# Kernel optimization log

Measured on AMD Instinct MI355X. Metric: run time of the kernel, lower is better.

## Reference

```python
import jax, jax.numpy as jnp
import numpy as np

N_NODES = 1_000_000
N_EDGES = 16_000_000
F_IN, F_H1, F_H2, N_CLS = 32, 16, 8, 5
N_GRAPHS = 10_000


def setup_inputs() -> dict:
    key = jax.random.key(0)
    ks = jax.random.split(key, 10)
    x = jax.random.normal(ks[0], (N_NODES, F_IN), dtype=jnp.float32)
    edge_index = jax.random.randint(ks[1], (2, N_EDGES), 0, N_NODES, dtype=jnp.int32)
    batch = jnp.sort(jax.random.randint(ks[2], (N_NODES,), 0, N_GRAPHS, dtype=jnp.int32))
    # learned params (Glorot-ish scale)
    W1 = jax.random.normal(ks[3], (F_IN, F_H1), dtype=jnp.float32) / np.sqrt(F_IN)
    b1 = jnp.zeros((F_H1,), dtype=jnp.float32)
    W2 = jax.random.normal(ks[4], (F_H1, F_H2), dtype=jnp.float32) / np.sqrt(F_H1)
    b2 = jnp.zeros((F_H2,), dtype=jnp.float32)
    Wl = jax.random.normal(ks[5], (F_H2, N_CLS), dtype=jnp.float32) / np.sqrt(F_H2)
    bl = jnp.zeros((N_CLS,), dtype=jnp.float32)
    return {"x": x, "edge_index": edge_index, "batch": batch, "num_graphs": N_GRAPHS,
            "W1": W1, "b1": b1, "W2": W2, "b2": b2, "Wl": Wl, "bl": bl}


def _gcn_conv(x, W, b, src, dst, deg_inv_sqrt, norm_e, num_nodes):
    # h = X W, then symmetric-normalized aggregation with self loops:
    # out_i = sum_{(j->i)} norm_ji * h_j + deg_i^{-1} * h_i + b
    h = x @ W                                  # [N, F_out]
    msg = h[src] * norm_e[:, None]             # [E, F_out] gather + scale
    agg = jax.ops.segment_sum(msg, dst, num_segments=num_nodes)
    self_loop = h * (deg_inv_sqrt * deg_inv_sqrt)[:, None]
    return agg + self_loop + b


def reference(x, edge_index, batch, num_graphs, W1, b1, W2, b2, Wl, bl):
    num_nodes = x.shape[0]
    src, dst = edge_index[0], edge_index[1]
    # degrees including self loops (GCN: A_hat = A + I)
    deg = jax.ops.segment_sum(jnp.ones_like(dst, dtype=x.dtype), dst,
                              num_segments=num_nodes) + 1.0
    deg_inv_sqrt = jax.lax.rsqrt(deg)
    norm_e = deg_inv_sqrt[src] * deg_inv_sqrt[dst]   # [E]

    h = _gcn_conv(x, W1, b1, src, dst, deg_inv_sqrt, norm_e, num_nodes)
    h = jax.nn.relu(h)
    h = _gcn_conv(h, W2, b2, src, dst, deg_inv_sqrt, norm_e, num_nodes)
    h = jax.nn.relu(h)

    # global_mean_pool over graph ids
    sums = jax.ops.segment_sum(h, batch, num_segments=num_graphs)     # [G, F_H2]
    cnts = jax.ops.segment_sum(jnp.ones((num_nodes,), dtype=h.dtype), batch,
                               num_segments=num_graphs)
    pooled = sums / jnp.maximum(cnts, 1.0)[:, None]
    return pooled @ Wl + bl
```

## Files before the change

kernel.cpp:

```cpp
#include <hip/hip_runtime.h>


namespace {

constexpr int F_IN = 32, F_H1 = 16, F_H2 = 8, N_CLS = 5;
constexpr int BB = 10, NPB = 1 << BB;
constexpr int MAXB = 1024;
constexpr int CHUNK = 12288;


__global__ void k_mm1(const float* __restrict__ x, const float* __restrict__ W,
                      float* __restrict__ h, int N) {
  __shared__ float w[F_IN * F_H1];
  for (int k = threadIdx.x; k < F_IN * F_H1; k += blockDim.x) w[k] = W[k];
  __syncthreads();
  int i = blockIdx.x * blockDim.x + threadIdx.x;
  if (i >= N) return;
  const float4* xr = reinterpret_cast<const float4*>(x + (size_t)i * F_IN);
  float acc[F_H1];
#pragma unroll
  for (int f = 0; f < F_H1; ++f) acc[f] = 0.f;
#pragma unroll
  for (int k4 = 0; k4 < F_IN / 4; ++k4) {
    float4 v = xr[k4];
    float vv[4] = {v.x, v.y, v.z, v.w};
#pragma unroll
    for (int j = 0; j < 4; ++j) {
      const float* wr = &w[(k4 * 4 + j) * F_H1];
#pragma unroll
      for (int f = 0; f < F_H1; ++f) acc[f] = fmaf(vv[j], wr[f], acc[f]);
    }
  }
  float4* hr = reinterpret_cast<float4*>(h + (size_t)i * F_H1);
#pragma unroll
  for (int q = 0; q < F_H1 / 4; ++q)
    hr[q] = make_float4(acc[q * 4], acc[q * 4 + 1], acc[q * 4 + 2], acc[q * 4 + 3]);
}

__global__ void k_mm2(const float* __restrict__ in, const float* __restrict__ W,
                      float* __restrict__ h, int N) {
  __shared__ float w[F_H1 * F_H2];
  for (int k = threadIdx.x; k < F_H1 * F_H2; k += blockDim.x) w[k] = W[k];
  __syncthreads();
  int i = blockIdx.x * blockDim.x + threadIdx.x;
  if (i >= N) return;
  const float4* xr = reinterpret_cast<const float4*>(in + (size_t)i * F_H1);
  float acc[F_H2];
#pragma unroll
  for (int f = 0; f < F_H2; ++f) acc[f] = 0.f;
#pragma unroll
  for (int k4 = 0; k4 < F_H1 / 4; ++k4) {
    float4 v = xr[k4];
    float vv[4] = {v.x, v.y, v.z, v.w};
#pragma unroll
    for (int j = 0; j < 4; ++j) {
      const float* wr = &w[(k4 * 4 + j) * F_H2];
#pragma unroll
      for (int f = 0; f < F_H2; ++f) acc[f] = fmaf(vv[j], wr[f], acc[f]);
    }
  }
  float4* hr = reinterpret_cast<float4*>(h + (size_t)i * F_H2);
#pragma unroll
  for (int q = 0; q < F_H2 / 4; ++q)
    hr[q] = make_float4(acc[q * 4], acc[q * 4 + 1], acc[q * 4 + 2], acc[q * 4 + 3]);
}

__global__ void k_final(const float* __restrict__ pooled, const float* __restrict__ cnts,
                        const float* __restrict__ Wl, const float* __restrict__ bl,
                        float* __restrict__ out, int total) {
  int gid = blockIdx.x * blockDim.x + threadIdx.x;
  if (gid >= total) return;
  int g = gid / N_CLS, c = gid % N_CLS;
  float s = 0.f;
#pragma unroll
  for (int f = 0; f < F_H2; ++f) s += pooled[g * F_H2 + f] * Wl[f * N_CLS + c];
  out[gid] = s / fmaxf(cnts[g], 1.f) + bl[c];
}


__global__ void k_hist(const int* __restrict__ dst, int* __restrict__ bcnt,
                       int E, int nbuck) {
  __shared__ int h[MAXB];
  for (int i = threadIdx.x; i < MAXB; i += blockDim.x) h[i] = 0;
  __syncthreads();
  for (int e = blockIdx.x * blockDim.x + threadIdx.x; e < E;
       e += gridDim.x * blockDim.x)
    atomicAdd(&h[dst[e] >> BB], 1);
  __syncthreads();
  for (int i = threadIdx.x; i < nbuck; i += blockDim.x)
    if (h[i]) atomicAdd(&bcnt[i], h[i]);
}

__global__ void k_bscan(const int* __restrict__ bcnt, int* __restrict__ bbase,
                        int* __restrict__ bcur, int nbuck, int E) {
  __shared__ int s[MAXB];
  int t = threadIdx.x;
  int v = (t < nbuck) ? bcnt[t] : 0;
  s[t] = v;
  __syncthreads();
  for (int off = 1; off < MAXB; off <<= 1) {
    int x = (t >= off) ? s[t - off] : 0;
    __syncthreads();
    s[t] += x;
    __syncthreads();
  }
  int ex = s[t] - v;
  if (t < nbuck) { bbase[t] = ex; bcur[t] = ex; }
  if (t == 0) bbase[nbuck] = E;
}

__global__ __launch_bounds__(256)
void k_binscatter(const int* __restrict__ dst, const int* __restrict__ src,
                  int* __restrict__ bcur, int* __restrict__ packed, int E) {
  __shared__ int hist[MAXB];
  __shared__ int sbase[MAXB];
  __shared__ int lcur[MAXB];
  __shared__ int stg[CHUNK];
  __shared__ int stmp[256];
  int t = threadIdx.x;
  int c0 = blockIdx.x * CHUNK;
  int n = min(CHUNK, E - c0);
  for (int i = t; i < MAXB; i += 256) hist[i] = 0;
  __syncthreads();
  for (int j = t; j < n; j += 256) atomicAdd(&hist[dst[c0 + j] >> BB], 1);
  __syncthreads();
  int v[4], sum = 0;
  int b4 = t * 4;
#pragma unroll
  for (int k = 0; k < 4; ++k) { v[k] = hist[b4 + k]; sum += v[k]; }
  stmp[t] = sum;
  __syncthreads();
  for (int off = 1; off < 256; off <<= 1) {
    int x = (t >= off) ? stmp[t - off] : 0;
    __syncthreads();
    stmp[t] += x;
    __syncthreads();
  }
  int run = stmp[t] - sum;
#pragma unroll
  for (int k = 0; k < 4; ++k) { sbase[b4 + k] = run; lcur[b4 + k] = run; run += v[k]; }
  __syncthreads();
  for (int i = t; i < MAXB; i += 256) {
    int c = hist[i];
    if (c) hist[i] = atomicAdd(&bcur[i], c);
  }
  __syncthreads();
  for (int j = t; j < n; j += 256) {
    int d = dst[c0 + j], s = src[c0 + j];
    int b = d >> BB;
    int p = atomicAdd(&lcur[b], 1);
    stg[p] = ((d & (NPB - 1)) << 20) | s;
  }
  __syncthreads();
  for (int j = t; j < n; j += 256) {
    int lo = 0, hi = MAXB - 1;
    while (lo < hi) {
      int mid = (lo + hi + 1) >> 1;
      if (sbase[mid] <= j) lo = mid; else hi = mid - 1;
    }
    packed[hist[lo] + (j - sbase[lo])] = stg[j];
  }
}

__global__ void k_dis_b(const int* __restrict__ bbase, const int* __restrict__ packed,
                        float* __restrict__ dis, int N) {
  __shared__ int cnt[NPB];
  int t = threadIdx.x;
  for (int i = t; i < NPB; i += blockDim.x) cnt[i] = 0;
  __syncthreads();
  int b = blockIdx.x;
  int beg = bbase[b], end = bbase[b + 1];
  for (int e = beg + t; e < end; e += blockDim.x)
    atomicAdd(&cnt[packed[e] >> 20], 1);
  __syncthreads();
  int node0 = b << BB;
  for (int i = t; i < NPB; i += blockDim.x) {
    int node = node0 + i;
    if (node < N) dis[node] = rsqrtf((float)cnt[i] + 1.0f);
  }
}


template <int F>
__global__ __launch_bounds__(512)
void k_conv(const int* __restrict__ bbase, const int* __restrict__ packed,
            const float* __restrict__ dis, const float* __restrict__ h,
            const float* __restrict__ bias, float* __restrict__ out, int N) {
  __shared__ float acc[NPB * F];
  int t = threadIdx.x;
  for (int i = t; i < NPB * F; i += 512) acc[i] = 0.f;
  __syncthreads();
  int b = blockIdx.x;
  int beg = bbase[b], end = bbase[b + 1];
  const int EPI = 512 / F;
  int f = t % F, eg = t / F;
  for (int e = beg + eg; e < end; e += 2 * EPI) {
    int p0 = packed[e];
    int s0 = p0 & ((1 << 20) - 1), d0 = p0 >> 20;
    float m0 = dis[s0] * h[(size_t)s0 * F + f];
    int e1 = e + EPI;
    if (e1 < end) {
      int p1 = packed[e1];
      int s1 = p1 & ((1 << 20) - 1), d1 = p1 >> 20;
      float m1 = dis[s1] * h[(size_t)s1 * F + f];
      atomicAdd(&acc[d0 * F + f], m0);
      atomicAdd(&acc[d1 * F + f], m1);
    } else {
      atomicAdd(&acc[d0 * F + f], m0);
    }
  }
  __syncthreads();
  int node0 = b << BB;
  for (int i = t; i < NPB * F; i += 512) {
    int node = node0 + i / F;
    if (node >= N) continue;
    int ff = i % F;
    float di = dis[node];
    float v = fmaf(di, acc[i], fmaf(di * di, h[(size_t)node * F + ff], bias[ff]));
    out[(size_t)node * F + ff] = fmaxf(v, 0.f);
  }
}

__global__ __launch_bounds__(512)
void k_conv_pool(const int* __restrict__ bbase, const int* __restrict__ packed,
                 const float* __restrict__ dis, const float* __restrict__ h,
                 const float* __restrict__ bias, const int* __restrict__ batch,
                 float* __restrict__ pooled, float* __restrict__ cnts, int N) {
  constexpr int F = F_H2;
  __shared__ float acc[NPB * F];
  int t = threadIdx.x;
  for (int i = t; i < NPB * F; i += 512) acc[i] = 0.f;
  __syncthreads();
  int b = blockIdx.x;
  int beg = bbase[b], end = bbase[b + 1];
  const int EPI = 512 / F;
  int f = t % F, eg = t / F;
  for (int e = beg + eg; e < end; e += 2 * EPI) {
    int p0 = packed[e];
    int s0 = p0 & ((1 << 20) - 1), d0 = p0 >> 20;
    float m0 = dis[s0] * h[(size_t)s0 * F + f];
    int e1 = e + EPI;
    if (e1 < end) {
      int p1 = packed[e1];
      int s1 = p1 & ((1 << 20) - 1), d1 = p1 >> 20;
      float m1 = dis[s1] * h[(size_t)s1 * F + f];
      atomicAdd(&acc[d0 * F + f], m0);
      atomicAdd(&acc[d1 * F + f], m1);
    } else {
      atomicAdd(&acc[d0 * F + f], m0);
    }
  }
  __syncthreads();
  int node0 = b << BB;
  for (int i = t; i < NPB * F; i += 512) {
    int node = node0 + i / F;
    if (node >= N) continue;
    int ff = i % F;
    float di = dis[node];
    float v = fmaf(di, acc[i], fmaf(di * di, h[(size_t)node * F + ff], bias[ff]));
    v = fmaxf(v, 0.f);
    int g = batch[node];
    atomicAdd(&pooled[g * F_H2 + ff], v);
    if (ff == 0) atomicAdd(&cnts[g], 1.0f);
  }
}


__global__ void k_deg(const int* __restrict__ dst, float* __restrict__ deg, int E) {
  int e = blockIdx.x * blockDim.x + threadIdx.x;
  if (e < E) atomicAdd(&deg[dst[e]], 1.0f);
}
__global__ void k_dis(float* __restrict__ d, int N) {
  int i = blockIdx.x * blockDim.x + threadIdx.x;
  if (i < N) d[i] = rsqrtf(d[i] + 1.0f);
}
template <int F>
__global__ void k_edge(const int* __restrict__ src, const int* __restrict__ dst,
                       const float* __restrict__ dis, const float* __restrict__ h,
                       float* __restrict__ agg, int total) {
  int gid = blockIdx.x * blockDim.x + threadIdx.x;
  if (gid >= total) return;
  int e = gid / F, f = gid % F;
  int s = src[e], d = dst[e];
  atomicAdd(&agg[d * F + f], h[s * F + f] * dis[s] * dis[d]);
}
template <int F>
__global__ void k_combine(const float* __restrict__ h, const float* __restrict__ dis,
                          const float* __restrict__ b, float* __restrict__ agg, int total) {
  int gid = blockIdx.x * blockDim.x + threadIdx.x;
  if (gid >= total) return;
  int i = gid / F, f = gid % F;
  float di = dis[i];
  agg[gid] = fmaxf(agg[gid] + h[gid] * di * di + b[f], 0.f);
}
__global__ void k_combine_pool_fb(const float* __restrict__ h2, const float* __restrict__ agg2,
                                  const float* __restrict__ dis, const float* __restrict__ b,
                                  const int* __restrict__ batch, float* __restrict__ pooled,
                                  float* __restrict__ cnts, int total) {
  int gid = blockIdx.x * blockDim.x + threadIdx.x;
  if (gid >= total) return;
  int i = gid >> 3, f = gid & 7;
  float di = dis[i];
  float v = fmaxf(agg2[gid] + h2[gid] * di * di + b[f], 0.f);
  int g = batch[i];
  atomicAdd(&pooled[g * F_H2 + f], v);
  if (f == 0) atomicAdd(&cnts[g], 1.0f);
}

}

extern "C" void kernel_launch(void* const* d_in, const int* in_sizes, int n_in,
                              void* d_out, int out_size, void* d_ws, size_t ws_size,
                              hipStream_t stream) {
  const float* x   = (const float*)d_in[0];
  const int* ei    = (const int*)d_in[1];
  const int* batch = (const int*)d_in[2];
  const float* W1 = (const float*)d_in[4];
  const float* b1 = (const float*)d_in[5];
  const float* W2 = (const float*)d_in[6];
  const float* b2 = (const float*)d_in[7];
  const float* Wl = (const float*)d_in[8];
  const float* bl = (const float*)d_in[9];

  const int N = in_sizes[0] / F_IN;
  const int E = in_sizes[1] / 2;
  const int G = out_size / N_CLS;
  const int* src  = ei;
  const int* dstp = ei + E;

  const int BLK = 256;
  const int nbuck = (N + NPB - 1) >> BB;

  size_t need = (size_t)(3 * MAXB + 8) * 4
              + (size_t)E * 4
              + (size_t)N * 4
              + (size_t)N * F_H1 * 4
              + (size_t)N * F_H1 * 4
              + (size_t)G * (F_H2 + 1) * 4 + 1024;

  if (N <= (1 << 20) && nbuck <= MAXB && ws_size >= need) {
    char* p = (char*)d_ws;
    int*   bcnt   = (int*)p;    p += (size_t)MAXB * 4;
    int*   bbase  = (int*)p;    p += (size_t)(MAXB + 4) * 4;
    int*   bcur   = (int*)p;    p += (size_t)MAXB * 4;
    int*   packed = (int*)p;    p += (size_t)E * 4;
    float* dis    = (float*)p;  p += (size_t)N * 4;
    float* H      = (float*)p;  p += (size_t)N * F_H1 * 4;
    float* O      = (float*)p;  p += (size_t)N * F_H1 * 4;
    float* pooled = (float*)p;  p += (size_t)G * F_H2 * 4;
    float* cnts   = (float*)p;

    hipMemsetAsync(bcnt, 0, (size_t)MAXB * 4, stream);
    hipMemsetAsync(pooled, 0, ((size_t)G * F_H2 + G) * 4, stream);

    k_hist<<<2048, BLK, 0, stream>>>(dstp, bcnt, E, nbuck);
    k_bscan<<<1, MAXB, 0, stream>>>(bcnt, bbase, bcur, nbuck, E);
    k_binscatter<<<(E + CHUNK - 1) / CHUNK, BLK, 0, stream>>>(dstp, src, bcur, packed, E);
    k_dis_b<<<nbuck, BLK, 0, stream>>>(bbase, packed, dis, N);

    k_mm1<<<(N + BLK - 1) / BLK, BLK, 0, stream>>>(x, W1, H, N);
    k_conv<F_H1><<<nbuck, 512, 0, stream>>>(bbase, packed, dis, H, b1, O, N);
    k_mm2<<<(N + BLK - 1) / BLK, BLK, 0, stream>>>(O, W2, H, N);
    k_conv_pool<<<nbuck, 512, 0, stream>>>(bbase, packed, dis, H, b2, batch,
                                           pooled, cnts, N);

    k_final<<<(G * N_CLS + BLK - 1) / BLK, BLK, 0, stream>>>(
        pooled, cnts, Wl, bl, (float*)d_out, G * N_CLS);
    return;
  }

  float* ws = (float*)d_ws;
  float* dis    = ws;
  float* A      = ws + N;
  float* B      = A + (size_t)N * F_H1;
  float* h2     = A;
  float* agg2   = A + (size_t)N * F_H2;
  float* pooled = B + (size_t)N * F_H1;
  float* cnts   = pooled + (size_t)G * F_H2;

  hipMemsetAsync(dis, 0, (size_t)N * sizeof(float), stream);
  hipMemsetAsync(B, 0, (size_t)N * F_H1 * sizeof(float), stream);
  hipMemsetAsync(pooled, 0, ((size_t)G * F_H2 + G) * sizeof(float), stream);

  k_deg<<<(E + BLK - 1) / BLK, BLK, 0, stream>>>(dstp, dis, E);
  k_dis<<<(N + BLK - 1) / BLK, BLK, 0, stream>>>(dis, N);
  k_mm1<<<(N + BLK - 1) / BLK, BLK, 0, stream>>>(x, W1, A, N);
  k_edge<F_H1><<<(E * F_H1 + BLK - 1) / BLK, BLK, 0, stream>>>(src, dstp, dis, A, B, E * F_H1);
  k_combine<F_H1><<<(N * F_H1 + BLK - 1) / BLK, BLK, 0, stream>>>(A, dis, b1, B, N * F_H1);
  hipMemsetAsync(agg2, 0, (size_t)N * F_H2 * sizeof(float), stream);
  k_mm2<<<(N + BLK - 1) / BLK, BLK, 0, stream>>>(B, W2, h2, N);
  k_edge<F_H2><<<(E * F_H2 + BLK - 1) / BLK, BLK, 0, stream>>>(src, dstp, dis, h2, agg2, E * F_H2);
  k_combine_pool_fb<<<(N * F_H2 + BLK - 1) / BLK, BLK, 0, stream>>>(
      h2, agg2, dis, b2, batch, pooled, cnts, N * F_H2);
  k_final<<<(G * N_CLS + BLK - 1) / BLK, BLK, 0, stream>>>(
      pooled, cnts, Wl, bl, (float*)d_out, G * N_CLS);
}
```

Measured before the change: 2.881 ms.

## Prescale features by source degree norm, unroll edge gather, pool in shared memory

The matmul kernels now multiply each output row by deg^-1/2, so the conv edge loops no longer gather dis[src] per edge and the self-loop term becomes dis*(acc+hs). The edge loop is unrolled 8 ways, issuing all packed and feature loads before the shared-memory atomics to raise memory-level parallelism. The pooling step accumulates into a small shared-memory window of 32 graph ids before flushing to global atomics, cutting global atomic traffic. This changes the floating-point rounding order slightly and uses more registers per thread.

After: 3.345 ms. +16.1%, slower.

```diff
diff --git a/kernel.cpp b/kernel.cpp
--- a/kernel.cpp
+++ b/kernel.cpp
@@ -10,7 +10,7 @@
 
 
 __global__ void k_mm1(const float* __restrict__ x, const float* __restrict__ W,
-                      float* __restrict__ h, int N) {
+                      const float* __restrict__ dis, float* __restrict__ h, int N) {
   __shared__ float w[F_IN * F_H1];
   for (int k = threadIdx.x; k < F_IN * F_H1; k += blockDim.x) w[k] = W[k];
   __syncthreads();
@@ -31,14 +31,16 @@
       for (int f = 0; f < F_H1; ++f) acc[f] = fmaf(vv[j], wr[f], acc[f]);
     }
   }
+  float s = dis ? dis[i] : 1.0f;
   float4* hr = reinterpret_cast<float4*>(h + (size_t)i * F_H1);
 #pragma unroll
   for (int q = 0; q < F_H1 / 4; ++q)
-    hr[q] = make_float4(acc[q * 4], acc[q * 4 + 1], acc[q * 4 + 2], acc[q * 4 + 3]);
+    hr[q] = make_float4(s * acc[q * 4], s * acc[q * 4 + 1], s * acc[q * 4 + 2],
+                        s * acc[q * 4 + 3]);
 }
 
 __global__ void k_mm2(const float* __restrict__ in, const float* __restrict__ W,
-                      float* __restrict__ h, int N) {
+                      const float* __restrict__ dis, float* __restrict__ h, int N) {
   __shared__ float w[F_H1 * F_H2];
   for (int k = threadIdx.x; k < F_H1 * F_H2; k += blockDim.x) w[k] = W[k];
   __syncthreads();
@@ -59,10 +61,12 @@
       for (int f = 0; f < F_H2; ++f) acc[f] = fmaf(vv[j], wr[f], acc[f]);
     }
   }
+  float s = dis ? dis[i] : 1.0f;
   float4* hr = reinterpret_cast<float4*>(h + (size_t)i * F_H2);
 #pragma unroll
   for (int q = 0; q < F_H2 / 4; ++q)
-    hr[q] = make_float4(acc[q * 4], acc[q * 4 + 1], acc[q * 4 + 2], acc[q * 4 + 3]);
+    hr[q] = make_float4(s * acc[q * 4], s * acc[q * 4 + 1], s * acc[q * 4 + 2],
+                        s * acc[q * 4 + 3]);
 }
 
 __global__ void k_final(const float* __restrict__ pooled, const float* __restrict__ cnts,
@@ -184,7 +188,7 @@
 template <int F>
 __global__ __launch_bounds__(512)
 void k_conv(const int* __restrict__ bbase, const int* __restrict__ packed,
-            const float* __restrict__ dis, const float* __restrict__ h,
+            const float* __restrict__ dis, const float* __restrict__ hs,
             const float* __restrict__ bias, float* __restrict__ out, int N) {
   __shared__ float acc[NPB * F];
   int t = threadIdx.x;
@@ -194,20 +198,23 @@
   int beg = bbase[b], end = bbase[b + 1];
   const int EPI = 512 / F;
   int f = t % F, eg = t / F;
-  for (int e = beg + eg; e < end; e += 2 * EPI) {
-    int p0 = packed[e];
-    int s0 = p0 & ((1 << 20) - 1), d0 = p0 >> 20;
-    float m0 = dis[s0] * h[(size_t)s0 * F + f];
-    int e1 = e + EPI;
-    if (e1 < end) {
-      int p1 = packed[e1];
-      int s1 = p1 & ((1 << 20) - 1), d1 = p1 >> 20;
-      float m1 = dis[s1] * h[(size_t)s1 * F + f];
-      atomicAdd(&acc[d0 * F + f], m0);
-      atomicAdd(&acc[d1 * F + f], m1);
-    } else {
-      atomicAdd(&acc[d0 * F + f], m0);
-    }
+  constexpr int U = 8;
+  int e = beg + eg;
+  for (; e + (U - 1) * EPI < end; e += U * EPI) {
+    int p[U];
+    float m[U];
+#pragma unroll
+    for (int k = 0; k < U; ++k) p[k] = packed[e + k * EPI];
+#pragma unroll
+    for (int k = 0; k < U; ++k)
+      m[k] = hs[(size_t)(p[k] & 0xFFFFF) * F + f];
+#pragma unroll
+    for (int k = 0; k < U; ++k)
+      atomicAdd(&acc[(p[k] >> 20) * F + f], m[k]);
+  }
+  for (; e < end; e += EPI) {
+    int p = packed[e];
+    atomicAdd(&acc[(p >> 20) * F + f], hs[(size_t)(p & 0xFFFFF) * F + f]);
   }
   __syncthreads();
   int node0 = b << BB;
@@ -215,53 +222,79 @@
     int node = node0 + i / F;
     if (node >= N) continue;
     int ff = i % F;
-    float di = dis[node];
-    float v = fmaf(di, acc[i], fmaf(di * di, h[(size_t)node * F + ff], bias[ff]));
+    float v = fmaf(dis[node], acc[i] + hs[(size_t)node * F + ff], bias[ff]);
     out[(size_t)node * F + ff] = fmaxf(v, 0.f);
   }
 }
 
 __global__ __launch_bounds__(512)
 void k_conv_pool(const int* __restrict__ bbase, const int* __restrict__ packed,
-                 const float* __restrict__ dis, const float* __restrict__ h,
+                 const float* __restrict__ dis, const float* __restrict__ hs,
                  const float* __restrict__ bias, const int* __restrict__ batch,
-                 float* __restrict__ pooled, float* __restrict__ cnts, int N) {
+                 float* __restrict__ pooled, float* __restrict__ cnts, int N, int G) {
   constexpr int F = F_H2;
+  constexpr int GW = 32;
   __shared__ float acc[NPB * F];
+  __shared__ float pacc[GW * F];
+  __shared__ float pcnt[GW];
+  __shared__ int gmin_s;
   int t = threadIdx.x;
   for (int i = t; i < NPB * F; i += 512) acc[i] = 0.f;
-  __syncthreads();
+  for (int i = t; i < GW * F; i += 512) pacc[i] = 0.f;
+  if (t < GW) pcnt[t] = 0.f;
   int b = blockIdx.x;
+  int node0 = b << BB;
+  if (t == 0) gmin_s = batch[node0];
+  __syncthreads();
   int beg = bbase[b], end = bbase[b + 1];
   const int EPI = 512 / F;
   int f = t % F, eg = t / F;
-  for (int e = beg + eg; e < end; e += 2 * EPI) {
-    int p0 = packed[e];
-    int s0 = p0 & ((1 << 20) - 1), d0 = p0 >> 20;
-    float m0 = dis[s0] * h[(size_t)s0 * F + f];
-    int e1 = e + EPI;
-    if (e1 < end) {
-      int p1 = packed[e1];
-      int s1 = p1 & ((1 << 20) - 1), d1 = p1 >> 20;
-      float m1 = dis[s1] * h[(size_t)s1 * F + f];
-      atomicAdd(&acc[d0 * F + f], m0);
-      atomicAdd(&acc[d1 * F + f], m1);
-    } else {
-      atomicAdd(&acc[d0 * F + f], m0);
-    }
-  }
-  __syncthreads();
-  int node0 = b << BB;
+  constexpr int U = 8;
+  int e = beg + eg;
+  for (; e + (U - 1) * EPI < end; e += U * EPI) {
+    int p[U];
+    float m[U];
+#pragma unroll
+    for (int k = 0; k < U; ++k) p[k] = packed[e + k * EPI];
+#pragma unroll
+    for (int k = 0; k < U; ++k)
+      m[k] = hs[(size_t)(p[k] & 0xFFFFF) * F + f];
+#pragma unroll
+    for (int k = 0; k < U; ++k)
+      atomicAdd(&acc[(p[k] >> 20) * F + f], m[k]);
+  }
+  for (; e < end; e += EPI) {
+    int p = packed[e];
+    atomicAdd(&acc[(p >> 20) * F + f], hs[(size_t)(p & 0xFFFFF) * F + f]);
+  }
+  __syncthreads();
+  int gmin = gmin_s;
   for (int i = t; i < NPB * F; i += 512) {
     int node = node0 + i / F;
     if (node >= N) continue;
     int ff = i % F;
-    float di = dis[node];
-    float v = fmaf(di, acc[i], fmaf(di * di, h[(size_t)node * F + ff], bias[ff]));
+    float v = fmaf(dis[node], acc[i] + hs[(size_t)node * F + ff], bias[ff]);
     v = fmaxf(v, 0.f);
     int g = batch[node];
-    atomicAdd(&pooled[g * F_H2 + ff], v);
-    if (ff == 0) atomicAdd(&cnts[g], 1.0f);
+    int idx = g - gmin;
+    if (idx < GW) {
+      atomicAdd(&pacc[idx * F + ff], v);
+      if (ff == 0) atomicAdd(&pcnt[idx], 1.0f);
+    } else {
+      atomicAdd(&pooled[g * F + ff], v);
+      if (ff == 0) atomicAdd(&cnts[g], 1.0f);
+    }
+  }
+  __syncthreads();
+  for (int i = t; i < GW * F; i += 512) {
+    int g = gmin + i / F;
+    float v = pacc[i];
+    if (g < G && v != 0.f) atomicAdd(&pooled[g * F + i % F], v);
+  }
+  if (t < GW) {
+    int g = gmin + t;
+    float c = pcnt[t];
+    if (g < G && c > 0.f) atomicAdd(&cnts[g], c);
   }
 }
 
@@ -358,11 +391,11 @@
     k_binscatter<<<(E + CHUNK - 1) / CHUNK, BLK, 0, stream>>>(dstp, src, bcur, packed, E);
     k_dis_b<<<nbuck, BLK, 0, stream>>>(bbase, packed, dis, N);
 
-    k_mm1<<<(N + BLK - 1) / BLK, BLK, 0, stream>>>(x, W1, H, N);
+    k_mm1<<<(N + BLK - 1) / BLK, BLK, 0, stream>>>(x, W1, dis, H, N);
     k_conv<F_H1><<<nbuck, 512, 0, stream>>>(bbase, packed, dis, H, b1, O, N);
-    k_mm2<<<(N + BLK - 1) / BLK, BLK, 0, stream>>>(O, W2, H, N);
+    k_mm2<<<(N + BLK - 1) / BLK, BLK, 0, stream>>>(O, W2, dis, H, N);
     k_conv_pool<<<nbuck, 512, 0, stream>>>(bbase, packed, dis, H, b2, batch,
-                                           pooled, cnts, N);
+                                           pooled, cnts, N, G);
 
     k_final<<<(G * N_CLS + BLK - 1) / BLK, BLK, 0, stream>>>(
         pooled, cnts, Wl, bl, (float*)d_out, G * N_CLS);
@@ -384,11 +417,11 @@
 
   k_deg<<<(E + BLK - 1) / BLK, BLK, 0, stream>>>(dstp, dis, E);
   k_dis<<<(N + BLK - 1) / BLK, BLK, 0, stream>>>(dis, N);
-  k_mm1<<<(N + BLK - 1) / BLK, BLK, 0, stream>>>(x, W1, A, N);
+  k_mm1<<<(N + BLK - 1) / BLK, BLK, 0, stream>>>(x, W1, nullptr, A, N);
   k_edge<F_H1><<<(E * F_H1 + BLK - 1) / BLK, BLK, 0, stream>>>(src, dstp, dis, A, B, E * F_H1);
   k_combine<F_H1><<<(N * F_H1 + BLK - 1) / BLK, BLK, 0, stream>>>(A, dis, b1, B, N * F_H1);
   hipMemsetAsync(agg2, 0, (size_t)N * F_H2 * sizeof(float), stream);
-  k_mm2<<<(N + BLK - 1) / BLK, BLK, 0, stream>>>(B, W2, h2, N);
+  k_mm2<<<(N + BLK - 1) / BLK, BLK, 0, stream>>>(B, W2, nullptr, h2, N);
   k_edge<F_H2><<<(E * F_H2 + BLK - 1) / BLK, BLK, 0, stream>>>(src, dstp, dis, h2, agg2, E * F_H2);
   k_combine_pool_fb<<<(N * F_H2 + BLK - 1) / BLK, BLK, 0, stream>>>(
       h2, agg2, dis, b2, batch, pooled, cnts, N * F_H2);
```
